# Performance work log

Hardware: AMD Instinct MI355X
Metric: run time of the kernel (lower is better)

Reference implementation:

```python
import jax, jax.numpy as jnp
import numpy as np

BATCH = 1024


def setup_inputs() -> dict:
    key = jax.random.key(0)
    ks = jax.random.split(key, 8)
    piece_positions = jax.random.randint(ks[0], (BATCH, 64, 10), 0, 2) > 0  # bool occupancy
    king_positions = jax.random.randint(ks[1], (BATCH, 2), 0, 64, dtype=jnp.int32)
    input_weights = jax.random.randint(ks[2], (64, 641, 256), -32768, 32767, dtype=jnp.int16)
    input_bias = jnp.zeros((256,), dtype=jnp.int16)
    w1 = jax.random.randint(ks[3], (32, 512), -128, 127, dtype=jnp.int8)
    b1 = jnp.zeros((32,), dtype=jnp.int32)
    w2 = jax.random.randint(ks[4], (32, 32), -128, 127, dtype=jnp.int8)
    b2 = jnp.zeros((32,), dtype=jnp.int32)
    out_w = jax.random.randint(ks[5], (32,), -128, 127, dtype=jnp.int8)
    out_b = jnp.zeros((1,), dtype=jnp.int32)
    return {
        'piece_positions': piece_positions, 'king_positions': king_positions,
        'input_weights': input_weights, 'input_bias': input_bias,
        'w1': w1, 'b1': b1, 'w2': w2, 'b2': b2, 'out_w': out_w, 'out_b': out_b,
    }


def _fc(x, w, b):
    # int8 inputs/weights, int32 accumulate, floor-div 64, clamp to [0,127] -> int8
    y = x.astype(jnp.int32) @ w.T.astype(jnp.int32) + b
    y = jnp.floor_divide(y, 64)
    return jnp.clip(y, 0, 127).astype(jnp.int8)


def reference(piece_positions, king_positions, input_weights, input_bias,
              w1, b1, w2, b2, out_w, out_b):
    B = piece_positions.shape[0]
    pp = piece_positions.reshape(B, 640).astype(jnp.int32)  # flattened 64x10 HalfKP features

    def half(king_idx):
        wk = input_weights[king_idx]            # (B, 641, 256) gathered per-sample king table
        feats = wk[:, :640, :].astype(jnp.int32)
        kbias = wk[:, 640, :].astype(jnp.int32)
        return jnp.einsum('bf,bfd->bd', pp, feats) + kbias  # (B, 256)

    white = half(king_positions[:, 0])
    black = half(king_positions[:, 1])
    # int16 wraparound semantics of the original: accumulate in int32, mod-cast to int16
    acc = (white + black + input_bias.astype(jnp.int32)).astype(jnp.int16)

    x = jnp.clip(acc, 0, 127).astype(jnp.int8)
    x = jnp.concatenate([x, x], axis=1)  # (B, 512) side_to_move || other_side
    x = _fc(x, w1, b1)
    x = _fc(x, w2, b2)
    s = jnp.sum(x.astype(jnp.int32) * out_w.astype(jnp.int32)) + out_b  # scalar sum over batch too (as in source)
    return jnp.floor_divide(s, 16)  # shape (1,)
```

## Files before the change

kernel.cpp:

```cpp
#include <hip/hip_runtime.h>
#include <stdint.h>

#define NDIM  256
#define NFEAT 640
#define NROWS 641
#define SG    8
#define MAXG  16
#define MAXRPB 320

typedef unsigned short ushort4v __attribute__((ext_vector_type(4)));
typedef unsigned short ushort8v __attribute__((ext_vector_type(8)));

__global__ void nnue_bucket(const int* __restrict__ kp, const int* __restrict__ W32,
                            const int* __restrict__ pp32, int nslots,
                            int* __restrict__ ws,
                            int* __restrict__ king_start, int* __restrict__ slot_list,
                            int* __restrict__ slot_pos)
{
    __shared__ int cnt[64];
    __shared__ int off[64];
    const int t = threadIdx.x;
    if (t < 64) cnt[t] = 0;
    if (t == 0) {
        int raww = 0, rawpp = 0;
        for (int i = 0; i < 16; ++i) {
            const int v = W32[i];
            if (v > 32767 || v < -32768) raww = 1;
            const int u = pp32[i];
            if (u != 0 && u != 1) rawpp = 1;
        }
        ws[0] = 0; ws[1] = raww; ws[2] = rawpp;
    }
    __syncthreads();
    for (int s = t; s < nslots; s += 256) atomicAdd(&cnt[kp[s]], 1);
    __syncthreads();
    if (t == 0) {
        int run = 0;
        for (int k = 0; k < 64; ++k) { off[k] = run; king_start[k] = run; run += cnt[k]; }
        king_start[64] = run;
    }
    __syncthreads();
    for (int s = t; s < nslots; s += 256) {
        const int k = kp[s];
        const int pos = atomicAdd(&off[k], 1);
        slot_list[pos] = s;
        slot_pos[s] = pos;
    }
}

struct GatherLds {
    int samp[SG];
    unsigned mask[MAXRPB];
    unsigned red[4][SG][NDIM / 2];
};

template<bool RAWW, bool RAWPP>
__device__ __forceinline__ void gather_body(
    const void* __restrict__ ppv, const void* __restrict__ Wv,
    const int* __restrict__ king_start, const int* __restrict__ slot_list,
    unsigned short* __restrict__ partial, int nslots, int rp, GatherLds& sh)
{
    const int bid = blockIdx.x;
    const int k = bid & 63;
    const int rest = bid >> 6;
    const int p = rest & (rp - 1);
    const int gi = rest / rp;
    const int t = threadIdx.x, l = t & 63, g = t >> 6;

    const int s0 = king_start[k], s1 = king_start[k + 1];
    const int base = s0 + gi * SG;
    if (base >= s1) return;
    const int ns = min(SG, s1 - base);
    const unsigned emask = (ns >= 32) ? 0xFFFFFFFFu : ((1u << ns) - 1u);
    const int rpb = NFEAT / rp;
    const int r0 = p * rpb;

    if (t < SG) sh.samp[t] = slot_list[base + min(t, ns - 1)] >> 1;
    __syncthreads();

    for (int r = t; r < rpb; r += 256) {
        unsigned mm = 0;
        #pragma unroll
        for (int i = 0; i < SG; ++i) {
            const int s = sh.samp[i];
            int v;
            if (RAWPP) v = ((const uint8_t*)ppv)[(size_t)s * NFEAT + r0 + r];
            else       v = ((const int*)ppv)[(size_t)s * NFEAT + r0 + r];
            mm |= (v != 0 ? 1u : 0u) << i;
        }
        sh.mask[r] = mm & emask;
    }
    __syncthreads();

    ushort4v acc[SG];
    #pragma unroll
    for (int i = 0; i < SG; ++i) acc[i] = (ushort4v)0;

    const char* Wk = (const char*)Wv + (size_t)k * NROWS * NDIM * (RAWW ? 2 : 4);
    const int rows_per_wave = rpb / 4;
    const int lbeg = g * rows_per_wave;

    #pragma unroll 2
    for (int rr = 0; rr < rows_per_wave; ++rr) {
        const int lr = lbeg + rr;
        unsigned mm = sh.mask[lr];
        mm = __builtin_amdgcn_readfirstlane(mm);
        ushort4v w;
        if (RAWW) {
            w = *(const ushort4v*)(Wk + (size_t)(r0 + lr) * 512 + (size_t)l * 8);
        } else {
            const int4 u = *(const int4*)(Wk + (size_t)(r0 + lr) * 1024 + (size_t)l * 16);
            w.x = (unsigned short)u.x; w.y = (unsigned short)u.y;
            w.z = (unsigned short)u.z; w.w = (unsigned short)u.w;
        }
        #pragma unroll
        for (int i = 0; i < SG; ++i)
            if (mm & (1u << i)) acc[i] += w;
    }

    #pragma unroll
    for (int i = 0; i < SG; ++i)
        *(ushort4v*)&sh.red[g][i][2 * l] = acc[i];
    __syncthreads();

    const int i = t >> 5;
    const int j4 = (t & 31) * 4;
    if (i < ns) {
        ushort8v s = *(const ushort8v*)&sh.red[0][i][j4];
        #pragma unroll
        for (int g2 = 1; g2 < 4; ++g2) s += *(const ushort8v*)&sh.red[g2][i][j4];
        *(ushort8v*)&partial[((size_t)p * nslots + base + i) * NDIM + (size_t)(t & 31) * 8] = s;
    }
}

__global__ __launch_bounds__(256, 6) void nnue_gather(
    const void* __restrict__ pp, const void* __restrict__ W,
    const int* __restrict__ ws, const int* __restrict__ king_start,
    const int* __restrict__ slot_list, unsigned short* __restrict__ partial,
    int nslots, int rp)
{
    __shared__ GatherLds sh;
    const int raww = ws[1], rawpp = ws[2];
    if (raww) {
        if (rawpp) gather_body<true,  true >(pp, W, king_start, slot_list, partial, nslots, rp, sh);
        else       gather_body<true,  false>(pp, W, king_start, slot_list, partial, nslots, rp, sh);
    } else {
        if (rawpp) gather_body<false, true >(pp, W, king_start, slot_list, partial, nslots, rp, sh);
        else       gather_body<false, false>(pp, W, king_start, slot_list, partial, nslots, rp, sh);
    }
}

struct CombineLds {
    alignas(16) int8_t x[NDIM];
    int fc[256];
    alignas(4) int8_t x2[32];
};

template<bool RAWW>
__device__ __forceinline__ void combine_body(
    const unsigned short* __restrict__ partial, const int* __restrict__ slot_pos,
    const int* __restrict__ kp, const void* __restrict__ Wv,
    const void* __restrict__ ibv,
    const void* __restrict__ w1v, const int* __restrict__ b1,
    const void* __restrict__ w2v, const int* __restrict__ b2,
    const void* __restrict__ owv, int* __restrict__ ws, int nslots, int rp,
    CombineLds& sh)
{
    const int b = blockIdx.x;
    const int t = threadIdx.x;

    const int pos0 = slot_pos[2 * b + 0];
    const int pos1 = slot_pos[2 * b + 1];
    const int k0 = kp[2 * b + 0];
    const int k1 = kp[2 * b + 1];
    {
        unsigned tot = 0;
        for (int pi = 0; pi < rp; ++pi) {
            tot += partial[((size_t)pi * nslots + pos0) * NDIM + t];
            tot += partial[((size_t)pi * nslots + pos1) * NDIM + t];
        }
        if (RAWW) {
            const uint16_t* Wq = (const uint16_t*)Wv;
            tot += Wq[((size_t)k0 * NROWS + NFEAT) * NDIM + t];
            tot += Wq[((size_t)k1 * NROWS + NFEAT) * NDIM + t];
            tot += ((const uint16_t*)ibv)[t];
        } else {
            const int* Wq = (const int*)Wv;
            tot += (unsigned)Wq[((size_t)k0 * NROWS + NFEAT) * NDIM + t];
            tot += (unsigned)Wq[((size_t)k1 * NROWS + NFEAT) * NDIM + t];
            tot += (unsigned)((const int*)ibv)[t];
        }
        int v = (int)(int16_t)(uint16_t)tot;
        v = v < 0 ? 0 : (v > 127 ? 127 : v);
        sh.x[t] = (int8_t)v;
    }
    __syncthreads();

    {
        const int o = t >> 3, part = t & 7;
        int y = 0;
        const uint32_t* xw = (const uint32_t*)sh.x;
        if (RAWW) {
            const uint32_t* w1r = (const uint32_t*)((const char*)w1v + o * 512);
            #pragma unroll
            for (int i = 0; i < 8; ++i) {
                const int wi = part * 8 + i;
                const uint32_t xv = xw[wi];
                const uint32_t wa = w1r[wi];
                const uint32_t wb = w1r[64 + wi];
                #pragma unroll
                for (int jj = 0; jj < 4; ++jj) {
                    const int xj  = (int)((xv >> (8 * jj)) & 0xFFu);
                    const int waj = (int)(int8_t)(uint8_t)(wa >> (8 * jj));
                    const int wbj = (int)(int8_t)(uint8_t)(wb >> (8 * jj));
                    y += xj * (waj + wbj);
                }
            }
        } else {
            const int* w1r = (const int*)w1v + o * 512;
            #pragma unroll
            for (int i = 0; i < 8; ++i) {
                const int wi = part * 8 + i;
                const uint32_t xv = xw[wi];
                #pragma unroll
                for (int jj = 0; jj < 4; ++jj) {
                    const int xj = (int)((xv >> (8 * jj)) & 0xFFu);
                    y += xj * (w1r[wi * 4 + jj] + w1r[256 + wi * 8 / 2 + jj]);
                }
            }
        }
        sh.fc[t] = y;
    }
    __syncthreads();

    if (t < 32) {
        int y = b1[t];
        #pragma unroll
        for (int pq = 0; pq < 8; ++pq) y += sh.fc[t * 8 + pq];
        y >>= 6;
        y = y < 0 ? 0 : (y > 127 ? 127 : y);
        sh.x2[t] = (int8_t)y;
    }
    __syncthreads();

    if (t < 32) {
        int y = b2[t];
        const uint32_t* x2w = (const uint32_t*)sh.x2;
        if (RAWW) {
            const uint32_t* w2r = (const uint32_t*)((const char*)w2v + t * 32);
            #pragma unroll
            for (int i = 0; i < 8; ++i) {
                const uint32_t xv = x2w[i];
                const uint32_t wv = w2r[i];
                #pragma unroll
                for (int jj = 0; jj < 4; ++jj)
                    y += (int)((xv >> (8 * jj)) & 0xFFu) * (int)(int8_t)(uint8_t)(wv >> (8 * jj));
            }
        } else {
            const int* w2r = (const int*)w2v + t * 32;
            #pragma unroll
            for (int i = 0; i < 8; ++i) {
                const uint32_t xv = x2w[i];
                #pragma unroll
                for (int jj = 0; jj < 4; ++jj)
                    y += (int)((xv >> (8 * jj)) & 0xFFu) * w2r[i * 4 + jj];
            }
        }
        y >>= 6;
        y = y < 0 ? 0 : (y > 127 ? 127 : y);
        const int owx = RAWW ? (int)((const int8_t*)owv)[t] : ((const int*)owv)[t];
        int pr = y * owx;
        #pragma unroll
        for (int off = 16; off > 0; off >>= 1) pr += __shfl_down(pr, off, 32);
        if (t == 0) atomicAdd(ws, pr);
    }
}

__global__ __launch_bounds__(256) void nnue_combine(
    const unsigned short* __restrict__ partial, const int* __restrict__ slot_pos,
    const int* __restrict__ kp, const void* __restrict__ W,
    const void* __restrict__ ib,
    const void* __restrict__ w1, const int* __restrict__ b1,
    const void* __restrict__ w2, const int* __restrict__ b2,
    const void* __restrict__ ow, int* __restrict__ ws, int nslots, int rp)
{
    __shared__ CombineLds sh;
    if (ws[1]) combine_body<true >(partial, slot_pos, kp, W, ib, w1, b1, w2, b2, ow, ws, nslots, rp, sh);
    else       combine_body<false>(partial, slot_pos, kp, W, ib, w1, b1, w2, b2, ow, ws, nslots, rp, sh);
}

__global__ void nnue_finalize(const int* __restrict__ ws, const int* __restrict__ ob,
                              int* __restrict__ out) {
    out[0] = (ws[0] + ob[0]) >> 4;
}

struct SharedBuf {
    uint8_t pp[NFEAT];
    int     acc[4][NDIM];
    alignas(16) int8_t x[NDIM];
    int     fc[256];
    alignas(4) int8_t x2[32];
    int     list[4][160];
};

__global__ void detect_layout(const int* __restrict__ W32, const int* __restrict__ pp32,
                              int* __restrict__ ws) {
    int raww = 0, rawpp = 0;
    for (int i = 0; i < 16; ++i) {
        const int v = W32[i];
        if (v > 32767 || v < -32768) raww = 1;
        const int u = pp32[i];
        if (u != 0 && u != 1) rawpp = 1;
    }
    ws[0] = 0; ws[1] = raww; ws[2] = rawpp;
}

template<bool RAWW, bool RAWPP>
__device__ __forceinline__ void mono_body(
    const void* __restrict__ ppv, const int* __restrict__ kp,
    const void* __restrict__ Wv,  const void* __restrict__ ibv,
    const void* __restrict__ w1v, const int* __restrict__ b1,
    const void* __restrict__ w2v, const int* __restrict__ b2,
    const void* __restrict__ owv, int* __restrict__ ws, SharedBuf& sh)
{
    const int b = blockIdx.x;
    const int t = threadIdx.x;
    const int l = t & 63;
    const int g = t >> 6;

    if (RAWPP) {
        const uint32_t* src = (const uint32_t*)((const uint8_t*)ppv + (size_t)b * NFEAT);
        if (t < NFEAT / 4) ((uint32_t*)sh.pp)[t] = src[t];
    } else {
        const int* src = (const int*)ppv + (size_t)b * NFEAT;
        for (int i = t; i < NFEAT; i += 256) sh.pp[i] = (uint8_t)(src[i] != 0);
    }
    __syncthreads();

    const int base = g * 160;
    int cnt = 0;
    for (int c = 0; c < 160; c += 64) {
        const int idx = c + l;
        const bool flag = (idx < 160) && (sh.pp[base + idx] != 0);
        const unsigned long long mmask = __ballot(flag);
        const int pos = cnt + (int)__popcll(mmask & ((1ull << l) - 1ull));
        if (flag) sh.list[g][pos] = base + idx;
        cnt += (int)__popcll(mmask);
    }

    const int k0 = kp[b * 2 + 0];
    const int k1 = kp[b * 2 + 1];
    int a0 = 0, a1 = 0, a2 = 0, a3 = 0, a4 = 0, a5 = 0, a6 = 0, a7 = 0;

    if (RAWW) {
        const char* W0 = (const char*)Wv + (size_t)k0 * (NROWS * NDIM * 2);
        const char* W1 = (const char*)Wv + (size_t)k1 * (NROWS * NDIM * 2);
        const int lo = l * 8;
        auto step = [&](int f) {
            const uint2 u0 = *(const uint2*)(W0 + f * 512 + lo);
            const uint2 u1 = *(const uint2*)(W1 + f * 512 + lo);
            a0 += (int)(u0.x & 0xFFFFu); a1 += (int)(u0.x >> 16);
            a2 += (int)(u0.y & 0xFFFFu); a3 += (int)(u0.y >> 16);
            a4 += (int)(u1.x & 0xFFFFu); a5 += (int)(u1.x >> 16);
            a6 += (int)(u1.y & 0xFFFFu); a7 += (int)(u1.y >> 16);
        };
        int j = 0;
        for (; j + 4 <= cnt; j += 4) {
            const int f0 = sh.list[g][j], f1 = sh.list[g][j + 1];
            const int f2 = sh.list[g][j + 2], f3 = sh.list[g][j + 3];
            step(f0); step(f1); step(f2); step(f3);
        }
        for (; j < cnt; ++j) step(sh.list[g][j]);
    } else {
        const char* W0 = (const char*)Wv + (size_t)k0 * (NROWS * NDIM * 4);
        const char* W1 = (const char*)Wv + (size_t)k1 * (NROWS * NDIM * 4);
        const int lo = l * 16;
        auto step = [&](int f) {
            const int4 u0 = *(const int4*)(W0 + f * 1024 + lo);
            const int4 u1 = *(const int4*)(W1 + f * 1024 + lo);
            a0 += u0.x; a1 += u0.y; a2 += u0.z; a3 += u0.w;
            a4 += u1.x; a5 += u1.y; a6 += u1.z; a7 += u1.w;
        };
        int j = 0;
        for (; j + 4 <= cnt; j += 4) {
            const int f0 = sh.list[g][j], f1 = sh.list[g][j + 1];
            const int f2 = sh.list[g][j + 2], f3 = sh.list[g][j + 3];
            step(f0); step(f1); step(f2); step(f3);
        }
        for (; j < cnt; ++j) step(sh.list[g][j]);
    }

    sh.acc[g][4 * l + 0] = a0 + a4;
    sh.acc[g][4 * l + 1] = a1 + a5;
    sh.acc[g][4 * l + 2] = a2 + a6;
    sh.acc[g][4 * l + 3] = a3 + a7;
    __syncthreads();

    {
        const int d = t;
        int tot = sh.acc[0][d] + sh.acc[1][d] + sh.acc[2][d] + sh.acc[3][d];
        int kb0, kb1, ibx;
        if (RAWW) {
            const int16_t* Wq = (const int16_t*)Wv;
            kb0 = Wq[((size_t)k0 * NROWS + NFEAT) * NDIM + d];
            kb1 = Wq[((size_t)k1 * NROWS + NFEAT) * NDIM + d];
            ibx = ((const int16_t*)ibv)[d];
        } else {
            const int* Wq = (const int*)Wv;
            kb0 = Wq[((size_t)k0 * NROWS + NFEAT) * NDIM + d];
            kb1 = Wq[((size_t)k1 * NROWS + NFEAT) * NDIM + d];
            ibx = ((const int*)ibv)[d];
        }
        tot += kb0 + kb1 + ibx;
        int v = (int)(int16_t)(uint16_t)(uint32_t)tot;
        v = v < 0 ? 0 : (v > 127 ? 127 : v);
        sh.x[d] = (int8_t)v;
    }
    __syncthreads();

    {
        const int o = t >> 3, part = t & 7;
        int y = 0;
        const uint32_t* xw = (const uint32_t*)sh.x;
        if (RAWW) {
            const uint32_t* w1r = (const uint32_t*)((const char*)w1v + o * 512);
            #pragma unroll
            for (int i = 0; i < 8; ++i) {
                const int wi = part * 8 + i;
                const uint32_t xv = xw[wi];
                const uint32_t wa = w1r[wi];
                const uint32_t wb = w1r[64 + wi];
                #pragma unroll
                for (int jj = 0; jj < 4; ++jj) {
                    const int xj  = (int)((xv >> (8 * jj)) & 0xFFu);
                    const int waj = (int)(int8_t)(uint8_t)(wa >> (8 * jj));
                    const int wbj = (int)(int8_t)(uint8_t)(wb >> (8 * jj));
                    y += xj * (waj + wbj);
                }
            }
        } else {
            const int* w1r = (const int*)w1v + o * 512;
            #pragma unroll
            for (int i = 0; i < 8; ++i) {
                const int wi = part * 8 + i;
                const uint32_t xv = xw[wi];
                #pragma unroll
                for (int jj = 0; jj < 4; ++jj) {
                    const int xj = (int)((xv >> (8 * jj)) & 0xFFu);
                    y += xj * (w1r[wi * 4 + jj] + w1r[256 + wi * 4 + jj]);
                }
            }
        }
        sh.fc[t] = y;
    }
    __syncthreads();

    if (t < 32) {
        int y = b1[t];
        #pragma unroll
        for (int pq = 0; pq < 8; ++pq) y += sh.fc[t * 8 + pq];
        y >>= 6;
        y = y < 0 ? 0 : (y > 127 ? 127 : y);
        sh.x2[t] = (int8_t)y;
    }
    __syncthreads();

    if (t < 32) {
        int y = b2[t];
        const uint32_t* x2w = (const uint32_t*)sh.x2;
        if (RAWW) {
            const uint32_t* w2r = (const uint32_t*)((const char*)w2v + t * 32);
            #pragma unroll
            for (int i = 0; i < 8; ++i) {
                const uint32_t xv = x2w[i];
                const uint32_t wv = w2r[i];
                #pragma unroll
                for (int jj = 0; jj < 4; ++jj)
                    y += (int)((xv >> (8 * jj)) & 0xFFu) * (int)(int8_t)(uint8_t)(wv >> (8 * jj));
            }
        } else {
            const int* w2r = (const int*)w2v + t * 32;
            #pragma unroll
            for (int i = 0; i < 8; ++i) {
                const uint32_t xv = x2w[i];
                #pragma unroll
                for (int jj = 0; jj < 4; ++jj)
                    y += (int)((xv >> (8 * jj)) & 0xFFu) * w2r[i * 4 + jj];
            }
        }
        y >>= 6;
        y = y < 0 ? 0 : (y > 127 ? 127 : y);
        const int owx = RAWW ? (int)((const int8_t*)owv)[t] : ((const int*)owv)[t];
        int pr = y * owx;
        #pragma unroll
        for (int off = 16; off > 0; off >>= 1) pr += __shfl_down(pr, off, 32);
        if (t == 0) atomicAdd(ws, pr);
    }
}

__global__ __launch_bounds__(256, 4) void nnue_mono(
    const void* __restrict__ pp, const int* __restrict__ kp,
    const void* __restrict__ W,  const void* __restrict__ ib,
    const void* __restrict__ w1, const int* __restrict__ b1,
    const void* __restrict__ w2, const int* __restrict__ b2,
    const void* __restrict__ ow, int* __restrict__ ws)
{
    __shared__ SharedBuf sh;
    const int raww = ws[1], rawpp = ws[2];
    if (raww) {
        if (rawpp) mono_body<true,  true >(pp, kp, W, ib, w1, b1, w2, b2, ow, ws, sh);
        else       mono_body<true,  false>(pp, kp, W, ib, w1, b1, w2, b2, ow, ws, sh);
    } else {
        if (rawpp) mono_body<false, true >(pp, kp, W, ib, w1, b1, w2, b2, ow, ws, sh);
        else       mono_body<false, false>(pp, kp, W, ib, w1, b1, w2, b2, ow, ws, sh);
    }
}

extern "C" void kernel_launch(void* const* d_in, const int* in_sizes, int n_in,
                              void* d_out, int out_size, void* d_ws, size_t ws_size,
                              hipStream_t stream)
{
    const void* pp = d_in[0];
    const int*  kp = (const int*)d_in[1];
    const void* W  = d_in[2];
    const void* ib = d_in[3];
    const void* w1 = d_in[4];
    const int*  b1 = (const int*)d_in[5];
    const void* w2 = d_in[6];
    const int*  b2 = (const int*)d_in[7];
    const void* ow = d_in[8];
    const int*  ob = (const int*)d_in[9];
    int* ws  = (int*)d_ws;
    int* out = (int*)d_out;

    const int B = in_sizes[1] / 2;
    const int nslots = 2 * B;

    const size_t off_ks = 16;
    const size_t off_sl = 96;
    const size_t off_sp = off_sl + (size_t)nslots;
    const size_t off_pb = ((off_sp + (size_t)nslots + 255) / 256) * 256;
    const size_t need4 = (off_pb + (size_t)4 * nslots * (NDIM / 2)) * 4;
    const size_t need2 = (off_pb + (size_t)2 * nslots * (NDIM / 2)) * 4;

    int rp = 0;
    if (ws_size >= need4) rp = 4;
    else if (ws_size >= need2) rp = 2;

    if (rp) {
        int* king_start = ws + off_ks;
        int* slot_list  = ws + off_sl;
        int* slot_pos   = ws + off_sp;
        unsigned short* partial = (unsigned short*)(ws + off_pb);

        hipLaunchKernelGGL(nnue_bucket, dim3(1), dim3(256), 0, stream,
                           kp, (const int*)W, (const int*)pp, nslots,
                           ws, king_start, slot_list, slot_pos);
        hipLaunchKernelGGL(nnue_gather, dim3(64 * MAXG * rp), dim3(256), 0, stream,
                           pp, W, ws, king_start, slot_list, partial, nslots, rp);
        hipLaunchKernelGGL(nnue_combine, dim3(B), dim3(256), 0, stream,
                           partial, slot_pos, kp, W, ib, w1, b1, w2, b2, ow, ws, nslots, rp);
        hipLaunchKernelGGL(nnue_finalize, dim3(1), dim3(1), 0, stream, ws, ob, out);
    } else {
        hipLaunchKernelGGL(detect_layout, dim3(1), dim3(1), 0, stream,
                           (const int*)W, (const int*)pp, ws);
        hipLaunchKernelGGL(nnue_mono, dim3(B), dim3(256), 0, stream,
                           pp, kp, W, ib, w1, b1, w2, b2, ow, ws);
        hipLaunchKernelGGL(nnue_finalize, dim3(1), dim3(1), 0, stream, ws, ob, out);
    }
}
```

Before: 143.5 us.

## Fuse bucket, gather, combine and finalize into one cooperative persistent kernel

Replaces the four-launch pipeline (bucket sort, gather, combine, finalize) with a single cooperative kernel that uses grid-wide syncs between phases. Each persistent block builds its own per-king sample list through ballot/popcount compaction instead of depending on a global bucket pass, then loops over virtual gather blocks and writes partials indexed directly by slot. The intent is to remove launch overhead and inter-kernel gaps. In exchange, every block redundantly scans all king indices, each list is capped at 512 entries, and the grid-wide barriers add their own cost.

```diff
diff --git a/kernel.cpp b/kernel.cpp
--- a/kernel.cpp
+++ b/kernel.cpp
@@ -1,183 +1,147 @@
 #include <hip/hip_runtime.h>
+#include <hip/hip_cooperative_groups.h>
 #include <stdint.h>
+
+namespace cg = cooperative_groups;
 
 #define NDIM  256
 #define NFEAT 640
 #define NROWS 641
 #define SG    8
-#define MAXG  16
-#define MAXRPB 320
+#define GRP   8
+#define RP    4
+#define VGRID 2048
+#define MAXLIST 512
 
 typedef unsigned short ushort4v __attribute__((ext_vector_type(4)));
 typedef unsigned short ushort8v __attribute__((ext_vector_type(8)));
 
-__global__ void nnue_bucket(const int* __restrict__ kp, const int* __restrict__ W32,
-                            const int* __restrict__ pp32, int nslots,
-                            int* __restrict__ ws,
-                            int* __restrict__ king_start, int* __restrict__ slot_list,
-                            int* __restrict__ slot_pos)
-{
-    __shared__ int cnt[64];
-    __shared__ int off[64];
-    const int t = threadIdx.x;
-    if (t < 64) cnt[t] = 0;
-    if (t == 0) {
-        int raww = 0, rawpp = 0;
-        for (int i = 0; i < 16; ++i) {
-            const int v = W32[i];
-            if (v > 32767 || v < -32768) raww = 1;
-            const int u = pp32[i];
-            if (u != 0 && u != 1) rawpp = 1;
-        }
-        ws[0] = 0; ws[1] = raww; ws[2] = rawpp;
-    }
-    __syncthreads();
-    for (int s = t; s < nslots; s += 256) atomicAdd(&cnt[kp[s]], 1);
-    __syncthreads();
-    if (t == 0) {
-        int run = 0;
-        for (int k = 0; k < 64; ++k) { off[k] = run; king_start[k] = run; run += cnt[k]; }
-        king_start[64] = run;
-    }
-    __syncthreads();
-    for (int s = t; s < nslots; s += 256) {
-        const int k = kp[s];
-        const int pos = atomicAdd(&off[k], 1);
-        slot_list[pos] = s;
-        slot_pos[s] = pos;
-    }
-}
-
-struct GatherLds {
+struct GaLds {
+    unsigned red[4][SG][NDIM / 2];
+    unsigned mask[160];
+    int list[MAXLIST];
+    int wcnt[4];
+    int cnt;
     int samp[SG];
-    unsigned mask[MAXRPB];
-    unsigned red[4][SG][NDIM / 2];
 };
+struct CbLds {
+    int8_t x[NDIM];
+    int fc[256];
+    int8_t x2[32];
+};
+#define SMEM_BYTES (sizeof(GaLds) > sizeof(CbLds) ? sizeof(GaLds) : sizeof(CbLds))
 
 template<bool RAWW, bool RAWPP>
-__device__ __forceinline__ void gather_body(
-    const void* __restrict__ ppv, const void* __restrict__ Wv,
-    const int* __restrict__ king_start, const int* __restrict__ slot_list,
-    unsigned short* __restrict__ partial, int nslots, int rp, GatherLds& sh)
-{
-    const int bid = blockIdx.x;
-    const int k = bid & 63;
-    const int rest = bid >> 6;
-    const int p = rest & (rp - 1);
-    const int gi = rest / rp;
+__device__ __forceinline__ void gather_vb(
+    int vb, bool first, const void* __restrict__ ppv, const int* __restrict__ kp,
+    const void* __restrict__ Wv, unsigned short* __restrict__ partial,
+    int nslots, GaLds* sh)
+{
     const int t = threadIdx.x, l = t & 63, g = t >> 6;
-
-    const int s0 = king_start[k], s1 = king_start[k + 1];
-    const int base = s0 + gi * SG;
-    if (base >= s1) return;
-    const int ns = min(SG, s1 - base);
-    const unsigned emask = (ns >= 32) ? 0xFFFFFFFFu : ((1u << ns) - 1u);
-    const int rpb = NFEAT / rp;
-    const int r0 = p * rpb;
-
-    if (t < SG) sh.samp[t] = slot_list[base + min(t, ns - 1)] >> 1;
-    __syncthreads();
-
-    for (int r = t; r < rpb; r += 256) {
-        unsigned mm = 0;
-        #pragma unroll
-        for (int i = 0; i < SG; ++i) {
-            const int s = sh.samp[i];
-            int v;
-            if (RAWPP) v = ((const uint8_t*)ppv)[(size_t)s * NFEAT + r0 + r];
-            else       v = ((const int*)ppv)[(size_t)s * NFEAT + r0 + r];
-            mm |= (v != 0 ? 1u : 0u) << i;
-        }
-        sh.mask[r] = mm & emask;
-    }
-    __syncthreads();
-
-    ushort4v acc[SG];
-    #pragma unroll
-    for (int i = 0; i < SG; ++i) acc[i] = (ushort4v)0;
-
+    const int k = vb & 63;
+    const int rest = vb >> 6;
+    const int p = rest & (RP - 1);
+    const int gi = rest / RP;
+
+    if (first) {
+        if (t == 0) sh->cnt = 0;
+        __syncthreads();
+        for (int c0 = 0; c0 < nslots; c0 += 256) {
+            const int s = c0 + t;
+            const bool f = (s < nslots) && (kp[s] == k);
+            const unsigned long long m = __ballot(f);
+            if (l == 0) sh->wcnt[g] = (int)__popcll(m);
+            __syncthreads();
+            int base = sh->cnt;
+            for (int w = 0; w < g; ++w) base += sh->wcnt[w];
+            const int pos = base + (int)__popcll(m & ((1ull << l) - 1ull));
+            if (f && pos < MAXLIST) sh->list[pos] = s;
+            __syncthreads();
+            if (t == 0) sh->cnt += sh->wcnt[0] + sh->wcnt[1] + sh->wcnt[2] + sh->wcnt[3];
+            __syncthreads();
+        }
+    }
+    const int cnt = min(sh->cnt, MAXLIST);
+    const int r0 = p * 160;
     const char* Wk = (const char*)Wv + (size_t)k * NROWS * NDIM * (RAWW ? 2 : 4);
-    const int rows_per_wave = rpb / 4;
-    const int lbeg = g * rows_per_wave;
-
-    #pragma unroll 2
-    for (int rr = 0; rr < rows_per_wave; ++rr) {
-        const int lr = lbeg + rr;
-        unsigned mm = sh.mask[lr];
-        mm = __builtin_amdgcn_readfirstlane(mm);
-        ushort4v w;
-        if (RAWW) {
-            w = *(const ushort4v*)(Wk + (size_t)(r0 + lr) * 512 + (size_t)l * 8);
-        } else {
-            const int4 u = *(const int4*)(Wk + (size_t)(r0 + lr) * 1024 + (size_t)l * 16);
-            w.x = (unsigned short)u.x; w.y = (unsigned short)u.y;
-            w.z = (unsigned short)u.z; w.w = (unsigned short)u.w;
-        }
+
+    for (int lbase = gi * SG; lbase < cnt; lbase += GRP * SG) {
+        const int ns = min(SG, cnt - lbase);
+        const unsigned emask = (1u << ns) - 1u;
+        if (t < SG) sh->samp[t] = sh->list[lbase + min(t, ns - 1)] >> 1;
+        __syncthreads();
+
+        for (int r = t; r < 160; r += 256) {
+            unsigned mm = 0;
+            #pragma unroll
+            for (int i = 0; i < SG; ++i) {
+                const int s = sh->samp[i];
+                int v;
+                if (RAWPP) v = ((const uint8_t*)ppv)[(size_t)s * NFEAT + r0 + r];
+                else       v = ((const int*)ppv)[(size_t)s * NFEAT + r0 + r];
+                mm |= (v != 0 ? 1u : 0u) << i;
+            }
+            sh->mask[r] = mm & emask;
+        }
+        __syncthreads();
+
+        ushort4v acc[SG];
+        #pragma unroll
+        for (int i = 0; i < SG; ++i) acc[i] = (ushort4v)0;
+
+        #pragma unroll 2
+        for (int rr = 0; rr < 40; ++rr) {
+            const int lr = g * 40 + rr;
+            unsigned mm = sh->mask[lr];
+            mm = __builtin_amdgcn_readfirstlane(mm);
+            ushort4v w;
+            if (RAWW) {
+                w = *(const ushort4v*)(Wk + (size_t)(r0 + lr) * 512 + (size_t)l * 8);
+            } else {
+                const int4 u = *(const int4*)(Wk + (size_t)(r0 + lr) * 1024 + (size_t)l * 16);
+                w.x = (unsigned short)u.x; w.y = (unsigned short)u.y;
+                w.z = (unsigned short)u.z; w.w = (unsigned short)u.w;
+            }
+            #pragma unroll
+            for (int i = 0; i < SG; ++i)
+                if (mm & (1u << i)) acc[i] += w;
+        }
+
         #pragma unroll
         for (int i = 0; i < SG; ++i)
-            if (mm & (1u << i)) acc[i] += w;
-    }
-
-    #pragma unroll
-    for (int i = 0; i < SG; ++i)
-        *(ushort4v*)&sh.red[g][i][2 * l] = acc[i];
-    __syncthreads();
-
-    const int i = t >> 5;
-    const int j4 = (t & 31) * 4;
-    if (i < ns) {
-        ushort8v s = *(const ushort8v*)&sh.red[0][i][j4];
-        #pragma unroll
-        for (int g2 = 1; g2 < 4; ++g2) s += *(const ushort8v*)&sh.red[g2][i][j4];
-        *(ushort8v*)&partial[((size_t)p * nslots + base + i) * NDIM + (size_t)(t & 31) * 8] = s;
-    }
-}
-
-__global__ __launch_bounds__(256, 6) void nnue_gather(
-    const void* __restrict__ pp, const void* __restrict__ W,
-    const int* __restrict__ ws, const int* __restrict__ king_start,
-    const int* __restrict__ slot_list, unsigned short* __restrict__ partial,
-    int nslots, int rp)
-{
-    __shared__ GatherLds sh;
-    const int raww = ws[1], rawpp = ws[2];
-    if (raww) {
-        if (rawpp) gather_body<true,  true >(pp, W, king_start, slot_list, partial, nslots, rp, sh);
-        else       gather_body<true,  false>(pp, W, king_start, slot_list, partial, nslots, rp, sh);
-    } else {
-        if (rawpp) gather_body<false, true >(pp, W, king_start, slot_list, partial, nslots, rp, sh);
-        else       gather_body<false, false>(pp, W, king_start, slot_list, partial, nslots, rp, sh);
-    }
-}
-
-struct CombineLds {
-    alignas(16) int8_t x[NDIM];
-    int fc[256];
-    alignas(4) int8_t x2[32];
-};
+            *(ushort4v*)&sh->red[g][i][2 * l] = acc[i];
+        __syncthreads();
+
+        const int i = t >> 5;
+        const int j4 = (t & 31) * 4;
+        if (i < ns) {
+            ushort8v s8 = *(const ushort8v*)&sh->red[0][i][j4];
+            #pragma unroll
+            for (int g2 = 1; g2 < 4; ++g2) s8 += *(const ushort8v*)&sh->red[g2][i][j4];
+            const int slot = sh->list[lbase + i];
+            *(ushort8v*)&partial[((size_t)p * nslots + slot) * NDIM + (size_t)(t & 31) * 8] = s8;
+        }
+        __syncthreads();
+    }
+}
 
 template<bool RAWW>
-__device__ __forceinline__ void combine_body(
-    const unsigned short* __restrict__ partial, const int* __restrict__ slot_pos,
-    const int* __restrict__ kp, const void* __restrict__ Wv,
-    const void* __restrict__ ibv,
+__device__ __forceinline__ void combine_one(
+    int b, const unsigned short* __restrict__ partial, const int* __restrict__ kp,
+    const void* __restrict__ Wv, const void* __restrict__ ibv,
     const void* __restrict__ w1v, const int* __restrict__ b1,
     const void* __restrict__ w2v, const int* __restrict__ b2,
-    const void* __restrict__ owv, int* __restrict__ ws, int nslots, int rp,
-    CombineLds& sh)
-{
-    const int b = blockIdx.x;
+    const void* __restrict__ owv, int* __restrict__ ws, int nslots, CbLds* sh)
+{
     const int t = threadIdx.x;
-
-    const int pos0 = slot_pos[2 * b + 0];
-    const int pos1 = slot_pos[2 * b + 1];
     const int k0 = kp[2 * b + 0];
     const int k1 = kp[2 * b + 1];
     {
         unsigned tot = 0;
-        for (int pi = 0; pi < rp; ++pi) {
-            tot += partial[((size_t)pi * nslots + pos0) * NDIM + t];
-            tot += partial[((size_t)pi * nslots + pos1) * NDIM + t];
+        #pragma unroll
+        for (int pi = 0; pi < RP; ++pi) {
+            tot += partial[((size_t)pi * nslots + 2 * b + 0) * NDIM + t];
+            tot += partial[((size_t)pi * nslots + 2 * b + 1) * NDIM + t];
         }
         if (RAWW) {
             const uint16_t* Wq = (const uint16_t*)Wv;
@@ -192,14 +156,14 @@
         }
         int v = (int)(int16_t)(uint16_t)tot;
         v = v < 0 ? 0 : (v > 127 ? 127 : v);
-        sh.x[t] = (int8_t)v;
+        sh->x[t] = (int8_t)v;
     }
     __syncthreads();
 
     {
         const int o = t >> 3, part = t & 7;
         int y = 0;
-        const uint32_t* xw = (const uint32_t*)sh.x;
+        const uint32_t* xw = (const uint32_t*)sh->x;
         if (RAWW) {
             const uint32_t* w1r = (const uint32_t*)((const char*)w1v + o * 512);
             #pragma unroll
@@ -225,27 +189,27 @@
                 #pragma unroll
                 for (int jj = 0; jj < 4; ++jj) {
                     const int xj = (int)((xv >> (8 * jj)) & 0xFFu);
-                    y += xj * (w1r[wi * 4 + jj] + w1r[256 + wi * 8 / 2 + jj]);
+                    y += xj * (w1r[wi * 4 + jj] + w1r[256 + wi * 4 + jj]);
                 }
             }
         }
-        sh.fc[t] = y;
+        sh->fc[t] = y;
     }
     __syncthreads();
 
     if (t < 32) {
         int y = b1[t];
         #pragma unroll
-        for (int pq = 0; pq < 8; ++pq) y += sh.fc[t * 8 + pq];
+        for (int pq = 0; pq < 8; ++pq) y += sh->fc[t * 8 + pq];
         y >>= 6;
         y = y < 0 ? 0 : (y > 127 ? 127 : y);
-        sh.x2[t] = (int8_t)y;
+        sh->x2[t] = (int8_t)y;
     }
     __syncthreads();
 
     if (t < 32) {
         int y = b2[t];
-        const uint32_t* x2w = (const uint32_t*)sh.x2;
+        const uint32_t* x2w = (const uint32_t*)sh->x2;
         if (RAWW) {
             const uint32_t* w2r = (const uint32_t*)((const char*)w2v + t * 32);
             #pragma unroll
@@ -274,24 +238,74 @@
         for (int off = 16; off > 0; off >>= 1) pr += __shfl_down(pr, off, 32);
         if (t == 0) atomicAdd(ws, pr);
     }
-}
-
-__global__ __launch_bounds__(256) void nnue_combine(
-    const unsigned short* __restrict__ partial, const int* __restrict__ slot_pos,
-    const int* __restrict__ kp, const void* __restrict__ W,
-    const void* __restrict__ ib,
-    const void* __restrict__ w1, const int* __restrict__ b1,
-    const void* __restrict__ w2, const int* __restrict__ b2,
-    const void* __restrict__ ow, int* __restrict__ ws, int nslots, int rp)
-{
-    __shared__ CombineLds sh;
-    if (ws[1]) combine_body<true >(partial, slot_pos, kp, W, ib, w1, b1, w2, b2, ow, ws, nslots, rp, sh);
-    else       combine_body<false>(partial, slot_pos, kp, W, ib, w1, b1, w2, b2, ow, ws, nslots, rp, sh);
-}
-
-__global__ void nnue_finalize(const int* __restrict__ ws, const int* __restrict__ ob,
-                              int* __restrict__ out) {
-    out[0] = (ws[0] + ob[0]) >> 4;
+    __syncthreads();
+}
+
+template<bool RAWW, bool RAWPP>
+__device__ __forceinline__ void run_all(
+    cg::grid_group& grid, char* smem,
+    const void* pp, const int* kp, const void* W, const void* ib,
+    const void* w1, const int* b1, const void* w2, const int* b2,
+    const void* ow, const int* ob, int* out, int* ws,
+    unsigned short* partial, int nslots)
+{
+    GaLds* ga = (GaLds*)smem;
+    CbLds* cb = (CbLds*)smem;
+
+    bool first = true;
+    for (int vb = blockIdx.x; vb < VGRID; vb += gridDim.x) {
+        gather_vb<RAWW, RAWPP>(vb, first, pp, kp, W, partial, nslots, ga);
+        first = false;
+    }
+    __threadfence();
+    grid.sync();
+
+    const int nsamp = nslots >> 1;
+    for (int b = blockIdx.x; b < nsamp; b += gridDim.x)
+        combine_one<RAWW>(b, partial, kp, W, ib, w1, b1, w2, b2, ow, ws, nslots, cb);
+    __threadfence();
+    grid.sync();
+
+    if (blockIdx.x == 0 && threadIdx.x == 0) {
+        const int s = __hip_atomic_load(ws, __ATOMIC_RELAXED, __HIP_MEMORY_SCOPE_AGENT);
+        out[0] = (s + ob[0]) >> 4;
+    }
+}
+
+__global__ __launch_bounds__(256, 8) void nnue_coop(
+    const void* pp, const int* kp, const void* W, const void* ib,
+    const void* w1, const int* b1, const void* w2, const int* b2,
+    const void* ow, const int* ob, int* out, int* ws,
+    unsigned short* partial, int nslots)
+{
+    cg::grid_group grid = cg::this_grid();
+    __shared__ __align__(16) char smem[SMEM_BYTES];
+    __shared__ int s_flags;
+
+    if (threadIdx.x == 0) {
+        int raww = 0, rawpp = 0;
+        const int* W32 = (const int*)W;
+        const int* pp32 = (const int*)pp;
+        for (int i = 0; i < 16; ++i) {
+            const int v = W32[i];
+            if (v > 32767 || v < -32768) raww = 1;
+            const int u = pp32[i];
+            if (u != 0 && u != 1) rawpp = 1;
+        }
+        s_flags = raww | (rawpp << 1);
+        if (blockIdx.x == 0)
+            __hip_atomic_store(ws, 0, __ATOMIC_RELAXED, __HIP_MEMORY_SCOPE_AGENT);
+    }
+    __syncthreads();
+    const int raww = s_flags & 1, rawpp = (s_flags >> 1) & 1;
+
+    if (raww) {
+        if (rawpp) run_all<true,  true >(grid, smem, pp, kp, W, ib, w1, b1, w2, b2, ow, ob, out, ws, partial, nslots);
+        else       run_all<true,  false>(grid, smem, pp, kp, W, ib, w1, b1, w2, b2, ow, ob, out, ws, partial, nslots);
+    } else {
+        if (rawpp) run_all<false, true >(grid, smem, pp, kp, W, ib, w1, b1, w2, b2, ow, ob, out, ws, partial, nslots);
+        else       run_all<false, false>(grid, smem, pp, kp, W, ib, w1, b1, w2, b2, ow, ob, out, ws, partial, nslots);
+    }
 }
 
 struct SharedBuf {
@@ -516,6 +530,11 @@
     }
 }
 
+__global__ void nnue_finalize(const int* __restrict__ ws, const int* __restrict__ ob,
+                              int* __restrict__ out) {
+    out[0] = (ws[0] + ob[0]) >> 4;
+}
+
 extern "C" void kernel_launch(void* const* d_in, const int* in_sizes, int n_in,
                               void* d_out, int out_size, void* d_ws, size_t ws_size,
                               hipStream_t stream)
@@ -533,35 +552,30 @@
     int* ws  = (int*)d_ws;
     int* out = (int*)d_out;
 
-    const int B = in_sizes[1] / 2;
-    const int nslots = 2 * B;
-
-    const size_t off_ks = 16;
-    const size_t off_sl = 96;
-    const size_t off_sp = off_sl + (size_t)nslots;
-    const size_t off_pb = ((off_sp + (size_t)nslots + 255) / 256) * 256;
-    const size_t need4 = (off_pb + (size_t)4 * nslots * (NDIM / 2)) * 4;
-    const size_t need2 = (off_pb + (size_t)2 * nslots * (NDIM / 2)) * 4;
-
-    int rp = 0;
-    if (ws_size >= need4) rp = 4;
-    else if (ws_size >= need2) rp = 2;
-
-    if (rp) {
-        int* king_start = ws + off_ks;
-        int* slot_list  = ws + off_sl;
-        int* slot_pos   = ws + off_sp;
-        unsigned short* partial = (unsigned short*)(ws + off_pb);
-
-        hipLaunchKernelGGL(nnue_bucket, dim3(1), dim3(256), 0, stream,
-                           kp, (const int*)W, (const int*)pp, nslots,
-                           ws, king_start, slot_list, slot_pos);
-        hipLaunchKernelGGL(nnue_gather, dim3(64 * MAXG * rp), dim3(256), 0, stream,
-                           pp, W, ws, king_start, slot_list, partial, nslots, rp);
-        hipLaunchKernelGGL(nnue_combine, dim3(B), dim3(256), 0, stream,
-                           partial, slot_pos, kp, W, ib, w1, b1, w2, b2, ow, ws, nslots, rp);
-        hipLaunchKernelGGL(nnue_finalize, dim3(1), dim3(1), 0, stream, ws, ob, out);
+    int nslots = 2 * (in_sizes[1] / 2);
+
+    unsigned short* partial = (unsigned short*)(ws + 64);
+    const size_t need = 64 * 4 + (size_t)RP * nslots * NDIM * 2;
+
+    int cus = 0, maxb = 0;
+    (void)hipDeviceGetAttribute(&cus, hipDeviceAttributeMultiprocessorCount, 0);
+    (void)hipOccupancyMaxActiveBlocksPerMultiprocessor(&maxb, (const void*)nnue_coop, 256, 0);
+    int grid = 0;
+    if (cus > 0 && maxb > 0) {
+        grid = maxb * cus;
+        if (grid > VGRID) grid = VGRID;
+        grid &= ~63;
+    }
+
+    if (ws_size >= need && grid >= 64) {
+        void* args[] = { (void*)&pp, (void*)&kp, (void*)&W, (void*)&ib,
+                         (void*)&w1, (void*)&b1, (void*)&w2, (void*)&b2,
+                         (void*)&ow, (void*)&ob, (void*)&out, (void*)&ws,
+                         (void*)&partial, (void*)&nslots };
+        hipLaunchCooperativeKernel((const void*)nnue_coop, dim3(grid), dim3(256),
+                                   args, 0, stream);
     } else {
+        const int B = nslots / 2;
         hipLaunchKernelGGL(detect_layout, dim3(1), dim3(1), 0, stream,
                            (const int*)W, (const int*)pp, ws);
         hipLaunchKernelGGL(nnue_mono, dim3(B), dim3(256), 0, stream,
```

Result: slower. 562.7 us (+292.2%).

## Restructure bucketed gather: 16-sample groups, per-wave partials, fused finalize

Applied to the files above, without the earlier changes.

The gather kernel now handles 16 samples per group and loops over groups within each king, so each weight row load is reused across more samples. The cross-wave LDS reduction is dropped: each wave writes its own partial (8 partial buffers total), and partials are indexed directly by slot, which removes slot_pos. The piece-occupancy loads are packed into 32-bit words and staged through LDS before the masks are built. The finalize kernel is folded into combine through a last-block atomic counter, saving one launch. In exchange, combine reads more partials, accumulator register pressure doubles, and the occupancy hint is removed.

```diff
diff --git a/kernel.cpp b/kernel.cpp
--- a/kernel.cpp
+++ b/kernel.cpp
@@ -4,18 +4,17 @@
 #define NDIM  256
 #define NFEAT 640
 #define NROWS 641
-#define SG    8
-#define MAXG  16
-#define MAXRPB 320
+#define SG    16
+#define MAXG  4
+#define RB    2
+#define PARTS 8
 
 typedef unsigned short ushort4v __attribute__((ext_vector_type(4)));
-typedef unsigned short ushort8v __attribute__((ext_vector_type(8)));
 
 __global__ void nnue_bucket(const int* __restrict__ kp, const int* __restrict__ W32,
                             const int* __restrict__ pp32, int nslots,
                             int* __restrict__ ws,
-                            int* __restrict__ king_start, int* __restrict__ slot_list,
-                            int* __restrict__ slot_pos)
+                            int* __restrict__ king_start, int* __restrict__ slot_list)
 {
     __shared__ int cnt[64];
     __shared__ int off[64];
@@ -29,7 +28,7 @@
             const int u = pp32[i];
             if (u != 0 && u != 1) rawpp = 1;
         }
-        ws[0] = 0; ws[1] = raww; ws[2] = rawpp;
+        ws[0] = 0; ws[1] = raww; ws[2] = rawpp; ws[3] = 0;
     }
     __syncthreads();
     for (int s = t; s < nslots; s += 256) atomicAdd(&cnt[kp[s]], 1);
@@ -44,113 +43,121 @@
         const int k = kp[s];
         const int pos = atomicAdd(&off[k], 1);
         slot_list[pos] = s;
-        slot_pos[s] = pos;
-    }
-}
-
-struct GatherLds {
-    int samp[SG];
-    unsigned mask[MAXRPB];
-    unsigned red[4][SG][NDIM / 2];
+    }
+}
+
+struct GaLds {
+    unsigned pps[SG][80];
+    unsigned mask[320];
+    int sslot[SG];
+    int ssamp[SG];
 };
 
 template<bool RAWW, bool RAWPP>
 __device__ __forceinline__ void gather_body(
     const void* __restrict__ ppv, const void* __restrict__ Wv,
     const int* __restrict__ king_start, const int* __restrict__ slot_list,
-    unsigned short* __restrict__ partial, int nslots, int rp, GatherLds& sh)
+    unsigned short* __restrict__ partial, int nslots, GaLds* sh)
 {
     const int bid = blockIdx.x;
     const int k = bid & 63;
     const int rest = bid >> 6;
-    const int p = rest & (rp - 1);
-    const int gi = rest / rp;
+    const int gi = rest & (MAXG - 1);
+    const int rb = rest >> 2;
     const int t = threadIdx.x, l = t & 63, g = t >> 6;
+    const int p = rb * 4 + g;
+    const int r0 = rb * 320;
 
     const int s0 = king_start[k], s1 = king_start[k + 1];
-    const int base = s0 + gi * SG;
-    if (base >= s1) return;
-    const int ns = min(SG, s1 - base);
-    const unsigned emask = (ns >= 32) ? 0xFFFFFFFFu : ((1u << ns) - 1u);
-    const int rpb = NFEAT / rp;
-    const int r0 = p * rpb;
-
-    if (t < SG) sh.samp[t] = slot_list[base + min(t, ns - 1)] >> 1;
-    __syncthreads();
-
-    for (int r = t; r < rpb; r += 256) {
-        unsigned mm = 0;
+    const int cnt = s1 - s0;
+    const char* Wk = (const char*)Wv + (size_t)k * NROWS * NDIM * (RAWW ? 2 : 4);
+
+    for (int lbase = gi * SG; lbase < cnt; lbase += MAXG * SG) {
+        const int ns = min(SG, cnt - lbase);
+        const unsigned emask = (ns >= 32) ? 0xFFFFu : ((1u << ns) - 1u) & 0xFFFFu;
+        if (t < SG) {
+            const int s = slot_list[s0 + lbase + min(t, ns - 1)];
+            sh->sslot[t] = s;
+            sh->ssamp[t] = s >> 1;
+        }
+        __syncthreads();
+
+        for (int j = t; j < SG * 80; j += 256) {
+            const int i = j / 80, c = j - i * 80;
+            const int s = sh->ssamp[i];
+            unsigned pk;
+            if (RAWPP) {
+                pk = *(const unsigned*)((const uint8_t*)ppv + (size_t)s * NFEAT + r0 + c * 4);
+            } else {
+                const int* q = (const int*)ppv + (size_t)s * NFEAT + r0 + c * 4;
+                pk = (unsigned)(q[0] != 0) | ((unsigned)(q[1] != 0) << 8)
+                   | ((unsigned)(q[2] != 0) << 16) | ((unsigned)(q[3] != 0) << 24);
+            }
+            sh->pps[i][c] = pk;
+        }
+        __syncthreads();
+
+        for (int r = t; r < 320; r += 256) {
+            const int q = r >> 2, sh8 = (r & 3) * 8;
+            unsigned mm = 0;
+            #pragma unroll
+            for (int i = 0; i < SG; ++i)
+                mm |= (((sh->pps[i][q] >> sh8) & 0xFFu) ? 1u : 0u) << i;
+            sh->mask[r] = mm & emask;
+        }
+        __syncthreads();
+
+        ushort4v acc[SG];
+        #pragma unroll
+        for (int i = 0; i < SG; ++i) acc[i] = (ushort4v)0;
+
+        #pragma unroll 2
+        for (int rr = 0; rr < 80; ++rr) {
+            const int lr = g * 80 + rr;
+            unsigned mm = sh->mask[lr];
+            mm = __builtin_amdgcn_readfirstlane(mm);
+            ushort4v w;
+            if (RAWW) {
+                w = *(const ushort4v*)(Wk + (size_t)(r0 + lr) * 512 + (size_t)l * 8);
+            } else {
+                const int4 u = *(const int4*)(Wk + (size_t)(r0 + lr) * 1024 + (size_t)l * 16);
+                w.x = (unsigned short)u.x; w.y = (unsigned short)u.y;
+                w.z = (unsigned short)u.z; w.w = (unsigned short)u.w;
+            }
+            #pragma unroll
+            for (int i = 0; i < SG; ++i)
+                if (mm & (1u << i)) acc[i] += w;
+        }
+
         #pragma unroll
         for (int i = 0; i < SG; ++i) {
-            const int s = sh.samp[i];
-            int v;
-            if (RAWPP) v = ((const uint8_t*)ppv)[(size_t)s * NFEAT + r0 + r];
-            else       v = ((const int*)ppv)[(size_t)s * NFEAT + r0 + r];
-            mm |= (v != 0 ? 1u : 0u) << i;
-        }
-        sh.mask[r] = mm & emask;
-    }
-    __syncthreads();
-
-    ushort4v acc[SG];
-    #pragma unroll
-    for (int i = 0; i < SG; ++i) acc[i] = (ushort4v)0;
-
-    const char* Wk = (const char*)Wv + (size_t)k * NROWS * NDIM * (RAWW ? 2 : 4);
-    const int rows_per_wave = rpb / 4;
-    const int lbeg = g * rows_per_wave;
-
-    #pragma unroll 2
-    for (int rr = 0; rr < rows_per_wave; ++rr) {
-        const int lr = lbeg + rr;
-        unsigned mm = sh.mask[lr];
-        mm = __builtin_amdgcn_readfirstlane(mm);
-        ushort4v w;
-        if (RAWW) {
-            w = *(const ushort4v*)(Wk + (size_t)(r0 + lr) * 512 + (size_t)l * 8);
-        } else {
-            const int4 u = *(const int4*)(Wk + (size_t)(r0 + lr) * 1024 + (size_t)l * 16);
-            w.x = (unsigned short)u.x; w.y = (unsigned short)u.y;
-            w.z = (unsigned short)u.z; w.w = (unsigned short)u.w;
-        }
-        #pragma unroll
-        for (int i = 0; i < SG; ++i)
-            if (mm & (1u << i)) acc[i] += w;
-    }
-
-    #pragma unroll
-    for (int i = 0; i < SG; ++i)
-        *(ushort4v*)&sh.red[g][i][2 * l] = acc[i];
-    __syncthreads();
-
-    const int i = t >> 5;
-    const int j4 = (t & 31) * 4;
-    if (i < ns) {
-        ushort8v s = *(const ushort8v*)&sh.red[0][i][j4];
-        #pragma unroll
-        for (int g2 = 1; g2 < 4; ++g2) s += *(const ushort8v*)&sh.red[g2][i][j4];
-        *(ushort8v*)&partial[((size_t)p * nslots + base + i) * NDIM + (size_t)(t & 31) * 8] = s;
-    }
-}
-
-__global__ __launch_bounds__(256, 6) void nnue_gather(
+            if (i < ns) {
+                const int slot = sh->sslot[i];
+                *(ushort4v*)&partial[((size_t)p * nslots + slot) * NDIM + 4 * l] = acc[i];
+            }
+        }
+        __syncthreads();
+    }
+}
+
+__global__ __launch_bounds__(256) void nnue_gather(
     const void* __restrict__ pp, const void* __restrict__ W,
     const int* __restrict__ ws, const int* __restrict__ king_start,
     const int* __restrict__ slot_list, unsigned short* __restrict__ partial,
-    int nslots, int rp)
-{
-    __shared__ GatherLds sh;
+    int nslots)
+{
+    __shared__ GaLds sh;
     const int raww = ws[1], rawpp = ws[2];
     if (raww) {
-        if (rawpp) gather_body<true,  true >(pp, W, king_start, slot_list, partial, nslots, rp, sh);
-        else       gather_body<true,  false>(pp, W, king_start, slot_list, partial, nslots, rp, sh);
+        if (rawpp) gather_body<true,  true >(pp, W, king_start, slot_list, partial, nslots, &sh);
+        else       gather_body<true,  false>(pp, W, king_start, slot_list, partial, nslots, &sh);
     } else {
-        if (rawpp) gather_body<false, true >(pp, W, king_start, slot_list, partial, nslots, rp, sh);
-        else       gather_body<false, false>(pp, W, king_start, slot_list, partial, nslots, rp, sh);
-    }
-}
-
-struct CombineLds {
+        if (rawpp) gather_body<false, true >(pp, W, king_start, slot_list, partial, nslots, &sh);
+        else       gather_body<false, false>(pp, W, king_start, slot_list, partial, nslots, &sh);
+    }
+}
+
+struct CbLds {
     alignas(16) int8_t x[NDIM];
     int fc[256];
     alignas(4) int8_t x2[32];
@@ -158,26 +165,23 @@
 
 template<bool RAWW>
 __device__ __forceinline__ void combine_body(
-    const unsigned short* __restrict__ partial, const int* __restrict__ slot_pos,
-    const int* __restrict__ kp, const void* __restrict__ Wv,
-    const void* __restrict__ ibv,
+    const unsigned short* __restrict__ partial, const int* __restrict__ kp,
+    const void* __restrict__ Wv, const void* __restrict__ ibv,
     const void* __restrict__ w1v, const int* __restrict__ b1,
     const void* __restrict__ w2v, const int* __restrict__ b2,
-    const void* __restrict__ owv, int* __restrict__ ws, int nslots, int rp,
-    CombineLds& sh)
+    const void* __restrict__ owv, const int* __restrict__ ob,
+    int* __restrict__ ws, int* __restrict__ out, int nslots, CbLds* sh)
 {
     const int b = blockIdx.x;
     const int t = threadIdx.x;
-
-    const int pos0 = slot_pos[2 * b + 0];
-    const int pos1 = slot_pos[2 * b + 1];
     const int k0 = kp[2 * b + 0];
     const int k1 = kp[2 * b + 1];
     {
         unsigned tot = 0;
-        for (int pi = 0; pi < rp; ++pi) {
-            tot += partial[((size_t)pi * nslots + pos0) * NDIM + t];
-            tot += partial[((size_t)pi * nslots + pos1) * NDIM + t];
+        #pragma unroll
+        for (int pi = 0; pi < PARTS; ++pi) {
+            tot += partial[((size_t)pi * nslots + 2 * b + 0) * NDIM + t];
+            tot += partial[((size_t)pi * nslots + 2 * b + 1) * NDIM + t];
         }
         if (RAWW) {
             const uint16_t* Wq = (const uint16_t*)Wv;
@@ -192,14 +196,14 @@
         }
         int v = (int)(int16_t)(uint16_t)tot;
         v = v < 0 ? 0 : (v > 127 ? 127 : v);
-        sh.x[t] = (int8_t)v;
+        sh->x[t] = (int8_t)v;
     }
     __syncthreads();
 
     {
         const int o = t >> 3, part = t & 7;
         int y = 0;
-        const uint32_t* xw = (const uint32_t*)sh.x;
+        const uint32_t* xw = (const uint32_t*)sh->x;
         if (RAWW) {
             const uint32_t* w1r = (const uint32_t*)((const char*)w1v + o * 512);
             #pragma unroll
@@ -225,27 +229,27 @@
                 #pragma unroll
                 for (int jj = 0; jj < 4; ++jj) {
                     const int xj = (int)((xv >> (8 * jj)) & 0xFFu);
-                    y += xj * (w1r[wi * 4 + jj] + w1r[256 + wi * 8 / 2 + jj]);
+                    y += xj * (w1r[wi * 4 + jj] + w1r[256 + wi * 4 + jj]);
                 }
             }
         }
-        sh.fc[t] = y;
+        sh->fc[t] = y;
     }
     __syncthreads();
 
     if (t < 32) {
         int y = b1[t];
         #pragma unroll
-        for (int pq = 0; pq < 8; ++pq) y += sh.fc[t * 8 + pq];
+        for (int pq = 0; pq < 8; ++pq) y += sh->fc[t * 8 + pq];
         y >>= 6;
         y = y < 0 ? 0 : (y > 127 ? 127 : y);
-        sh.x2[t] = (int8_t)y;
+        sh->x2[t] = (int8_t)y;
     }
     __syncthreads();
 
     if (t < 32) {
         int y = b2[t];
-        const uint32_t* x2w = (const uint32_t*)sh.x2;
+        const uint32_t* x2w = (const uint32_t*)sh->x2;
         if (RAWW) {
             const uint32_t* w2r = (const uint32_t*)((const char*)w2v + t * 32);
             #pragma unroll
@@ -272,26 +276,30 @@
         int pr = y * owx;
         #pragma unroll
         for (int off = 16; off > 0; off >>= 1) pr += __shfl_down(pr, off, 32);
-        if (t == 0) atomicAdd(ws, pr);
+        if (t == 0) {
+            atomicAdd(ws, pr);
+            __threadfence();
+            const int prev = atomicAdd(ws + 3, 1);
+            if (prev == (int)gridDim.x - 1) {
+                __threadfence();
+                const int s = atomicAdd(ws, 0);
+                out[0] = (s + ob[0]) >> 4;
+            }
+        }
     }
 }
 
 __global__ __launch_bounds__(256) void nnue_combine(
-    const unsigned short* __restrict__ partial, const int* __restrict__ slot_pos,
-    const int* __restrict__ kp, const void* __restrict__ W,
-    const void* __restrict__ ib,
+    const unsigned short* __restrict__ partial, const int* __restrict__ kp,
+    const void* __restrict__ W, const void* __restrict__ ib,
     const void* __restrict__ w1, const int* __restrict__ b1,
     const void* __restrict__ w2, const int* __restrict__ b2,
-    const void* __restrict__ ow, int* __restrict__ ws, int nslots, int rp)
-{
-    __shared__ CombineLds sh;
-    if (ws[1]) combine_body<true >(partial, slot_pos, kp, W, ib, w1, b1, w2, b2, ow, ws, nslots, rp, sh);
-    else       combine_body<false>(partial, slot_pos, kp, W, ib, w1, b1, w2, b2, ow, ws, nslots, rp, sh);
-}
-
-__global__ void nnue_finalize(const int* __restrict__ ws, const int* __restrict__ ob,
-                              int* __restrict__ out) {
-    out[0] = (ws[0] + ob[0]) >> 4;
+    const void* __restrict__ ow, const int* __restrict__ ob,
+    int* __restrict__ ws, int* __restrict__ out, int nslots)
+{
+    __shared__ CbLds sh;
+    if (ws[1]) combine_body<true >(partial, kp, W, ib, w1, b1, w2, b2, ow, ob, ws, out, nslots, &sh);
+    else       combine_body<false>(partial, kp, W, ib, w1, b1, w2, b2, ow, ob, ws, out, nslots, &sh);
 }
 
 struct SharedBuf {
@@ -516,6 +524,11 @@
     }
 }
 
+__global__ void nnue_finalize(const int* __restrict__ ws, const int* __restrict__ ob,
+                              int* __restrict__ out) {
+    out[0] = (ws[0] + ob[0]) >> 4;
+}
+
 extern "C" void kernel_launch(void* const* d_in, const int* in_sizes, int n_in,
                               void* d_out, int out_size, void* d_ws, size_t ws_size,
                               hipStream_t stream)
@@ -538,29 +551,21 @@
 
     const size_t off_ks = 16;
     const size_t off_sl = 96;
-    const size_t off_sp = off_sl + (size_t)nslots;
-    const size_t off_pb = ((off_sp + (size_t)nslots + 255) / 256) * 256;
-    const size_t need4 = (off_pb + (size_t)4 * nslots * (NDIM / 2)) * 4;
-    const size_t need2 = (off_pb + (size_t)2 * nslots * (NDIM / 2)) * 4;
-
-    int rp = 0;
-    if (ws_size >= need4) rp = 4;
-    else if (ws_size >= need2) rp = 2;
-
-    if (rp) {
+    const size_t off_pb = ((off_sl + (size_t)nslots + 255) / 256) * 256;
+    const size_t need   = (off_pb + (size_t)PARTS * nslots * (NDIM / 2)) * 4;
+
+    if (ws_size >= need) {
         int* king_start = ws + off_ks;
         int* slot_list  = ws + off_sl;
-        int* slot_pos   = ws + off_sp;
         unsigned short* partial = (unsigned short*)(ws + off_pb);
 
         hipLaunchKernelGGL(nnue_bucket, dim3(1), dim3(256), 0, stream,
                            kp, (const int*)W, (const int*)pp, nslots,
-                           ws, king_start, slot_list, slot_pos);
-        hipLaunchKernelGGL(nnue_gather, dim3(64 * MAXG * rp), dim3(256), 0, stream,
-                           pp, W, ws, king_start, slot_list, partial, nslots, rp);
+                           ws, king_start, slot_list);
+        hipLaunchKernelGGL(nnue_gather, dim3(64 * MAXG * RB), dim3(256), 0, stream,
+                           pp, W, ws, king_start, slot_list, partial, nslots);
         hipLaunchKernelGGL(nnue_combine, dim3(B), dim3(256), 0, stream,
-                           partial, slot_pos, kp, W, ib, w1, b1, w2, b2, ow, ws, nslots, rp);
-        hipLaunchKernelGGL(nnue_finalize, dim3(1), dim3(1), 0, stream, ws, ob, out);
+                           partial, kp, W, ib, w1, b1, w2, b2, ow, ob, ws, out, nslots);
     } else {
         hipLaunchKernelGGL(detect_layout, dim3(1), dim3(1), 0, stream,
                            (const int*)W, (const int*)pp, ws);
```

After: 166.8 us. 1.16x slower.
